# Kernel tuning notes

Hardware: AMD Instinct MI355X
Metric: run time of the kernel (lower is better)

The kernel has to match this reference:

```python
import jax, jax.numpy as jnp
import numpy as np

EPS = 1e-8  # matches PairwiseCosine eps clamp


def setup_inputs() -> dict:
    key = jax.random.key(0)
    k1, k2, k3 = jax.random.split(key, 3)
    B, N, M, D = 8, 2048, 2048, 256
    desc_src = jax.random.normal(k1, (B, N, D), dtype=jnp.float32)
    desc_dst = jax.random.normal(k2, (B, M, D), dtype=jnp.float32)
    points_dst = jax.random.uniform(k3, (B, M, 2), dtype=jnp.float32)
    return {"desc_src": desc_src, "desc_dst": desc_dst, "points_dst": points_dst}


def reference(desc_src, desc_dst, points_dst):
    # Pairwise cosine similarity: [B, N, M]
    xx = jnp.linalg.norm(desc_src, axis=-1, keepdims=True)          # [B, N, 1]
    yy = jnp.linalg.norm(desc_dst, axis=-1, keepdims=True)          # [B, M, 1]
    xy = jnp.einsum('bnd,bmd->bnm', desc_src, desc_dst)             # [B, N, M]
    sim = xy / jnp.maximum(xx * jnp.swapaxes(yy, 1, 2), EPS)
    # Best match per source descriptor
    confidence = jnp.max(sim, axis=2)                               # [B, N]
    idx = jnp.argmax(sim, axis=2)                                   # [B, N]
    # Gather matched destination points: [B, N, 2]
    matched = jnp.take_along_axis(points_dst, idx[:, :, None], axis=1)
    return (matched, confidence)
```

## Files before the change

kernel.cpp:

```cpp
#include <hip/hip_runtime.h>
#include <stdint.h>

constexpr int Bq = 8, Nq = 2048, Mq = 2048, Dq = 256;
constexpr int TILE = 128;
constexpr int KC = 32;
constexpr int NCH = Dq / KC;
constexpr int LDS_S = 40;

typedef float f32x4 __attribute__((ext_vector_type(4)));
typedef _Float16 f16x8 __attribute__((ext_vector_type(8)));
typedef __fp16 fp16x2 __attribute__((ext_vector_type(2)));

__device__ __forceinline__ uint32_t f2sortable(float f) {
  uint32_t u = __float_as_uint(f);
  return (u & 0x80000000u) ? ~u : (u | 0x80000000u);
}
__device__ __forceinline__ float sortable2f(uint32_t s) {
  uint32_t u = (s & 0x80000000u) ? (s ^ 0x80000000u) : ~s;
  return __uint_as_float(u);
}

__device__ __forceinline__ void load16(float* d, const float* __restrict__ p) {
  *(float4*)&d[0]  = *(const float4*)(p + 0);
  *(float4*)&d[4]  = *(const float4*)(p + 4);
  *(float4*)&d[8]  = *(const float4*)(p + 8);
  *(float4*)&d[12] = *(const float4*)(p + 12);
}

__device__ __forceinline__ void split8(const float* x, f16x8* hi, f16x8* lo,
                                       float& sq) {
  union { f16x8 v; fp16x2 p[4]; } H, L;
#pragma unroll
  for (int j = 0; j < 4; ++j) {
    float x0 = x[2 * j], x1 = x[2 * j + 1];
    sq = fmaf(x0, x0, sq);
    sq = fmaf(x1, x1, sq);
    float h0 = __uint_as_float(__float_as_uint(x0) & 0xFFFFE000u);
    float h1 = __uint_as_float(__float_as_uint(x1) & 0xFFFFE000u);
    H.p[j] = __builtin_amdgcn_cvt_pkrtz(h0, h1);
    L.p[j] = __builtin_amdgcn_cvt_pkrtz(x0 - h0, x1 - h1);
  }
  *hi = H.v;
  *lo = L.v;
}

__global__ __launch_bounds__(256, 3)
void simmax_kernel(const float* __restrict__ src, const float* __restrict__ dst,
                   unsigned long long* __restrict__ best) {
  __shared__ _Float16 Ah[TILE][LDS_S], Al[TILE][LDS_S];
  __shared__ _Float16 Bh[TILE][LDS_S], Bl[TILE][LDS_S];
  __shared__ float invnx_s[TILE], invny_s[TILE];

  const int b = blockIdx.z, nt = blockIdx.y, mt = blockIdx.x;
  const int tid = threadIdx.x;
  const int lane = tid & 63;
  const int wave = tid >> 6;
  const int wy = wave >> 1, wx = wave & 1;
  const int ln15 = lane & 15, lq = lane >> 4;

  const int sr = tid >> 1;
  const int sk = (tid & 1) * 16;
  const float* Ag = src + ((size_t)(b * Nq + nt * TILE + sr)) * Dq + sk;
  const float* Bg = dst + ((size_t)(b * Mq + mt * TILE + sr)) * Dq + sk;

  f32x4 acc[4][4];
#pragma unroll
  for (int i = 0; i < 4; ++i)
#pragma unroll
    for (int j = 0; j < 4; ++j) acc[i][j] = (f32x4){0.f, 0.f, 0.f, 0.f};
  float sqa = 0.f, sqb = 0.f;

  float av[16], bv[16];
  load16(av, Ag);
  load16(bv, Bg);

  for (int c = 0; c < NCH; ++c) {
    f16x8 ah2[2], al2[2], bh2[2], bl2[2];
    split8(&av[0], &ah2[0], &al2[0], sqa);
    split8(&av[8], &ah2[1], &al2[1], sqa);
    split8(&bv[0], &bh2[0], &bl2[0], sqb);
    split8(&bv[8], &bh2[1], &bl2[1], sqb);
    __syncthreads();
    *(f16x8*)&Ah[sr][sk]     = ah2[0];
    *(f16x8*)&Ah[sr][sk + 8] = ah2[1];
    *(f16x8*)&Al[sr][sk]     = al2[0];
    *(f16x8*)&Al[sr][sk + 8] = al2[1];
    *(f16x8*)&Bh[sr][sk]     = bh2[0];
    *(f16x8*)&Bh[sr][sk + 8] = bh2[1];
    *(f16x8*)&Bl[sr][sk]     = bl2[0];
    *(f16x8*)&Bl[sr][sk + 8] = bl2[1];
    __syncthreads();

    if (c + 1 < NCH) {
      load16(av, Ag + (c + 1) * KC);
      load16(bv, Bg + (c + 1) * KC);
    }

    f16x8 bhf[4], blf[4];
#pragma unroll
    for (int ct = 0; ct < 4; ++ct) {
      int rowb = wx * 64 + ct * 16 + ln15;
      bhf[ct] = *(const f16x8*)&Bh[rowb][lq * 8];
      blf[ct] = *(const f16x8*)&Bl[rowb][lq * 8];
    }
#pragma unroll
    for (int rt = 0; rt < 4; ++rt) {
      int rowa = wy * 64 + rt * 16 + ln15;
      f16x8 ahf = *(const f16x8*)&Ah[rowa][lq * 8];
      f16x8 alf = *(const f16x8*)&Al[rowa][lq * 8];
#pragma unroll
      for (int ct = 0; ct < 4; ++ct) {
        acc[rt][ct] = __builtin_amdgcn_mfma_f32_16x16x32_f16(ahf, bhf[ct], acc[rt][ct], 0, 0, 0);
        acc[rt][ct] = __builtin_amdgcn_mfma_f32_16x16x32_f16(ahf, blf[ct], acc[rt][ct], 0, 0, 0);
        acc[rt][ct] = __builtin_amdgcn_mfma_f32_16x16x32_f16(alf, bhf[ct], acc[rt][ct], 0, 0, 0);
      }
    }
  }

  sqa += __shfl_xor(sqa, 1);
  sqb += __shfl_xor(sqb, 1);
  if ((tid & 1) == 0) {
    invnx_s[sr] = 1.0f / sqrtf(sqa);
    invny_s[sr] = 1.0f / sqrtf(sqb);
  }
  __syncthreads();

  float invny[4];
#pragma unroll
  for (int ct = 0; ct < 4; ++ct) invny[ct] = invny_s[wx * 64 + ct * 16 + ln15];

#pragma unroll
  for (int rt = 0; rt < 4; ++rt) {
#pragma unroll
    for (int reg = 0; reg < 4; ++reg) {
      float bq = -1e30f;
      int bc = 0x7FFFFFFF;
#pragma unroll
      for (int ct = 0; ct < 4; ++ct) {
        float q = acc[rt][ct][reg] * invny[ct];
        int cg = mt * TILE + wx * 64 + ct * 16 + ln15;
        if (q > bq || (q == bq && cg < bc)) { bq = q; bc = cg; }
      }
#pragma unroll
      for (int m = 1; m <= 8; m <<= 1) {
        float q2 = __shfl_xor(bq, m);
        int c2 = __shfl_xor(bc, m);
        if (q2 > bq || (q2 == bq && c2 < bc)) { bq = q2; bc = c2; }
      }
      if (ln15 == 0) {
        int rloc = wy * 64 + rt * 16 + lq * 4 + reg;
        float conf = bq * invnx_s[rloc];
        unsigned long long p =
            ((unsigned long long)(f2sortable(conf) ^ 0x80000000u) << 32) |
            (uint32_t)(~(uint32_t)bc);
        atomicMax((long long*)&best[(size_t)b * Nq + nt * TILE + rloc],
                  (long long)p);
      }
    }
  }
}

__global__ void finalize_kernel(const unsigned long long* __restrict__ best,
                                const float* __restrict__ pts,
                                float* __restrict__ out) {
  int i = blockIdx.x * blockDim.x + threadIdx.x;
  if (i >= Bq * Nq) return;
  unsigned long long p = best[i];
  uint32_t s = (uint32_t)(p >> 32) ^ 0x80000000u;
  int idx = (int)(~(uint32_t)(p & 0xFFFFFFFFull));
  float conf = sortable2f(s);
  int b = i / Nq;
  const float* q = pts + ((size_t)b * Mq + (size_t)idx) * 2;
  out[(size_t)i * 2 + 0] = q[0];
  out[(size_t)i * 2 + 1] = q[1];
  out[(size_t)(Bq * Nq) * 2 + i] = conf;
}

extern "C" void kernel_launch(void* const* d_in, const int* in_sizes, int n_in,
                              void* d_out, int out_size, void* d_ws, size_t ws_size,
                              hipStream_t stream) {
  const float* src = (const float*)d_in[0];
  const float* dst = (const float*)d_in[1];
  const float* pts = (const float*)d_in[2];
  float* out = (float*)d_out;

  unsigned long long* best = (unsigned long long*)d_ws;

  {
    dim3 grid(Mq / TILE, Nq / TILE, Bq);
    simmax_kernel<<<grid, 256, 0, stream>>>(src, dst, best);
  }
  {
    int blocks = (Bq * Nq + 255) / 256;
    finalize_kernel<<<blocks, 256, 0, stream>>>(best, pts, out);
  }
}
```

Baseline: 150.2 us.

## Precompute fp16 hi/lo splits and norms in separate kernel, load via global_load_lds

```diff
diff --git a/kernel.cpp b/kernel.cpp
--- a/kernel.cpp
+++ b/kernel.cpp
@@ -5,12 +5,20 @@
 constexpr int TILE = 128;
 constexpr int KC = 32;
 constexpr int NCH = Dq / KC;
-constexpr int LDS_S = 40;
+constexpr size_t ROWS = (size_t)Bq * Nq;
+constexpr size_t ARR = ROWS * Dq;
 
 typedef float f32x4 __attribute__((ext_vector_type(4)));
 typedef _Float16 f16x8 __attribute__((ext_vector_type(8)));
 typedef __fp16 fp16x2 __attribute__((ext_vector_type(2)));
 
+typedef const __attribute__((address_space(1))) void* as1_t;
+typedef __attribute__((address_space(3))) void* as3_t;
+
+__device__ __forceinline__ void gl_lds16(const void* g, void* l) {
+  __builtin_amdgcn_global_load_lds((as1_t)g, (as3_t)l, 16, 0, 0);
+}
+
 __device__ __forceinline__ uint32_t f2sortable(float f) {
   uint32_t u = __float_as_uint(f);
   return (u & 0x80000000u) ? ~u : (u | 0x80000000u);
@@ -20,36 +28,48 @@
   return __uint_as_float(u);
 }
 
-__device__ __forceinline__ void load16(float* d, const float* __restrict__ p) {
-  *(float4*)&d[0]  = *(const float4*)(p + 0);
-  *(float4*)&d[4]  = *(const float4*)(p + 4);
-  *(float4*)&d[8]  = *(const float4*)(p + 8);
-  *(float4*)&d[12] = *(const float4*)(p + 12);
-}
-
-__device__ __forceinline__ void split8(const float* x, f16x8* hi, f16x8* lo,
-                                       float& sq) {
-  union { f16x8 v; fp16x2 p[4]; } H, L;
-#pragma unroll
-  for (int j = 0; j < 4; ++j) {
+__global__ __launch_bounds__(256)
+void split_kernel(const float* __restrict__ src, const float* __restrict__ dst,
+                  uint16_t* __restrict__ Ahg, uint16_t* __restrict__ Alg,
+                  uint16_t* __restrict__ Bhg, uint16_t* __restrict__ Blg,
+                  float* __restrict__ inv_ns, float* __restrict__ inv_nd) {
+  int w = blockIdx.x * 4 + (threadIdx.x >> 6);
+  int lane = threadIdx.x & 63;
+  bool isB = w >= (int)ROWS;
+  int row = isB ? (w - (int)ROWS) : w;
+  const float* p = (isB ? dst : src) + (size_t)row * Dq + lane * 4;
+  float4 v = *(const float4*)p;
+  float x[4] = {v.x, v.y, v.z, v.w};
+  float sq = 0.f;
+  union { fp16x2 p2[2]; uint2 u; } H, L;
+#pragma unroll
+  for (int j = 0; j < 2; ++j) {
     float x0 = x[2 * j], x1 = x[2 * j + 1];
     sq = fmaf(x0, x0, sq);
     sq = fmaf(x1, x1, sq);
     float h0 = __uint_as_float(__float_as_uint(x0) & 0xFFFFE000u);
     float h1 = __uint_as_float(__float_as_uint(x1) & 0xFFFFE000u);
-    H.p[j] = __builtin_amdgcn_cvt_pkrtz(h0, h1);
-    L.p[j] = __builtin_amdgcn_cvt_pkrtz(x0 - h0, x1 - h1);
-  }
-  *hi = H.v;
-  *lo = L.v;
-}
-
-__global__ __launch_bounds__(256, 3)
-void simmax_kernel(const float* __restrict__ src, const float* __restrict__ dst,
+    H.p2[j] = __builtin_amdgcn_cvt_pkrtz(h0, h1);
+    L.p2[j] = __builtin_amdgcn_cvt_pkrtz(x0 - h0, x1 - h1);
+  }
+  uint16_t* hp = (isB ? Bhg : Ahg) + (size_t)row * Dq + lane * 4;
+  uint16_t* lp = (isB ? Blg : Alg) + (size_t)row * Dq + lane * 4;
+  *(uint2*)hp = H.u;
+  *(uint2*)lp = L.u;
+#pragma unroll
+  for (int m = 32; m >= 1; m >>= 1) sq += __shfl_xor(sq, m);
+  if (lane == 0) {
+    float inv = 1.0f / sqrtf(sq);
+    (isB ? inv_nd : inv_ns)[row] = inv;
+  }
+}
+
+__global__ __launch_bounds__(256, 4)
+void simmax_kernel(const uint16_t* __restrict__ Ahg, const uint16_t* __restrict__ Alg,
+                   const uint16_t* __restrict__ Bhg, const uint16_t* __restrict__ Blg,
+                   const float* __restrict__ inv_ns, const float* __restrict__ inv_nd,
                    unsigned long long* __restrict__ best) {
-  __shared__ _Float16 Ah[TILE][LDS_S], Al[TILE][LDS_S];
-  __shared__ _Float16 Bh[TILE][LDS_S], Bl[TILE][LDS_S];
-  __shared__ float invnx_s[TILE], invny_s[TILE];
+  __shared__ __align__(16) _Float16 lds[4][TILE][KC];
 
   const int b = blockIdx.z, nt = blockIdx.y, mt = blockIdx.x;
   const int tid = threadIdx.x;
@@ -58,56 +78,39 @@
   const int wy = wave >> 1, wx = wave & 1;
   const int ln15 = lane & 15, lq = lane >> 4;
 
-  const int sr = tid >> 1;
-  const int sk = (tid & 1) * 16;
-  const float* Ag = src + ((size_t)(b * Nq + nt * TILE + sr)) * Dq + sk;
-  const float* Bg = dst + ((size_t)(b * Mq + mt * TILE + sr)) * Dq + sk;
+  const uint16_t* garr = (wave == 0) ? Ahg : (wave == 1) ? Alg
+                        : (wave == 2) ? Bhg : Blg;
+  const int rowg0 = (wave < 2) ? (b * Nq + nt * TILE) : (b * Mq + mt * TILE);
+  const int q = (lane & 3) ^ ((lane >> 3) & 3);
+  const uint16_t* gbase = garr + ((size_t)(rowg0 + (lane >> 2)) * Dq + q * 8);
 
   f32x4 acc[4][4];
 #pragma unroll
   for (int i = 0; i < 4; ++i)
 #pragma unroll
     for (int j = 0; j < 4; ++j) acc[i][j] = (f32x4){0.f, 0.f, 0.f, 0.f};
-  float sqa = 0.f, sqb = 0.f;
-
-  float av[16], bv[16];
-  load16(av, Ag);
-  load16(bv, Bg);
+
+  const int sl = (lq ^ ((ln15 >> 1) & 3)) * 8;
 
   for (int c = 0; c < NCH; ++c) {
-    f16x8 ah2[2], al2[2], bh2[2], bl2[2];
-    split8(&av[0], &ah2[0], &al2[0], sqa);
-    split8(&av[8], &ah2[1], &al2[1], sqa);
-    split8(&bv[0], &bh2[0], &bl2[0], sqb);
-    split8(&bv[8], &bh2[1], &bl2[1], sqb);
     __syncthreads();
-    *(f16x8*)&Ah[sr][sk]     = ah2[0];
-    *(f16x8*)&Ah[sr][sk + 8] = ah2[1];
-    *(f16x8*)&Al[sr][sk]     = al2[0];
-    *(f16x8*)&Al[sr][sk + 8] = al2[1];
-    *(f16x8*)&Bh[sr][sk]     = bh2[0];
-    *(f16x8*)&Bh[sr][sk + 8] = bh2[1];
-    *(f16x8*)&Bl[sr][sk]     = bl2[0];
-    *(f16x8*)&Bl[sr][sk + 8] = bl2[1];
+#pragma unroll
+    for (int t = 0; t < 8; ++t)
+      gl_lds16(gbase + (size_t)(16 * t) * Dq + c * KC, &lds[wave][16 * t][0]);
     __syncthreads();
-
-    if (c + 1 < NCH) {
-      load16(av, Ag + (c + 1) * KC);
-      load16(bv, Bg + (c + 1) * KC);
-    }
 
     f16x8 bhf[4], blf[4];
 #pragma unroll
     for (int ct = 0; ct < 4; ++ct) {
       int rowb = wx * 64 + ct * 16 + ln15;
-      bhf[ct] = *(const f16x8*)&Bh[rowb][lq * 8];
-      blf[ct] = *(const f16x8*)&Bl[rowb][lq * 8];
+      bhf[ct] = *(const f16x8*)&lds[2][rowb][sl];
+      blf[ct] = *(const f16x8*)&lds[3][rowb][sl];
     }
 #pragma unroll
     for (int rt = 0; rt < 4; ++rt) {
       int rowa = wy * 64 + rt * 16 + ln15;
-      f16x8 ahf = *(const f16x8*)&Ah[rowa][lq * 8];
-      f16x8 alf = *(const f16x8*)&Al[rowa][lq * 8];
+      f16x8 ahf = *(const f16x8*)&lds[0][rowa][sl];
+      f16x8 alf = *(const f16x8*)&lds[1][rowa][sl];
 #pragma unroll
       for (int ct = 0; ct < 4; ++ct) {
         acc[rt][ct] = __builtin_amdgcn_mfma_f32_16x16x32_f16(ahf, bhf[ct], acc[rt][ct], 0, 0, 0);
@@ -117,17 +120,10 @@
     }
   }
 
-  sqa += __shfl_xor(sqa, 1);
-  sqb += __shfl_xor(sqb, 1);
-  if ((tid & 1) == 0) {
-    invnx_s[sr] = 1.0f / sqrtf(sqa);
-    invny_s[sr] = 1.0f / sqrtf(sqb);
-  }
-  __syncthreads();
-
   float invny[4];
 #pragma unroll
-  for (int ct = 0; ct < 4; ++ct) invny[ct] = invny_s[wx * 64 + ct * 16 + ln15];
+  for (int ct = 0; ct < 4; ++ct)
+    invny[ct] = inv_nd[b * Mq + mt * TILE + wx * 64 + ct * 16 + ln15];
 
 #pragma unroll
   for (int rt = 0; rt < 4; ++rt) {
@@ -137,9 +133,9 @@
       int bc = 0x7FFFFFFF;
 #pragma unroll
       for (int ct = 0; ct < 4; ++ct) {
-        float q = acc[rt][ct][reg] * invny[ct];
+        float qv = acc[rt][ct][reg] * invny[ct];
         int cg = mt * TILE + wx * 64 + ct * 16 + ln15;
-        if (q > bq || (q == bq && cg < bc)) { bq = q; bc = cg; }
+        if (qv > bq || (qv == bq && cg < bc)) { bq = qv; bc = cg; }
       }
 #pragma unroll
       for (int m = 1; m <= 8; m <<= 1) {
@@ -149,7 +145,7 @@
       }
       if (ln15 == 0) {
         int rloc = wy * 64 + rt * 16 + lq * 4 + reg;
-        float conf = bq * invnx_s[rloc];
+        float conf = bq * inv_ns[b * Nq + nt * TILE + rloc];
         unsigned long long p =
             ((unsigned long long)(f2sortable(conf) ^ 0x80000000u) << 32) |
             (uint32_t)(~(uint32_t)bc);
@@ -164,16 +160,16 @@
                                 const float* __restrict__ pts,
                                 float* __restrict__ out) {
   int i = blockIdx.x * blockDim.x + threadIdx.x;
-  if (i >= Bq * Nq) return;
+  if (i >= (int)ROWS) return;
   unsigned long long p = best[i];
   uint32_t s = (uint32_t)(p >> 32) ^ 0x80000000u;
   int idx = (int)(~(uint32_t)(p & 0xFFFFFFFFull));
   float conf = sortable2f(s);
   int b = i / Nq;
-  const float* q = pts + ((size_t)b * Mq + (size_t)idx) * 2;
-  out[(size_t)i * 2 + 0] = q[0];
-  out[(size_t)i * 2 + 1] = q[1];
-  out[(size_t)(Bq * Nq) * 2 + i] = conf;
+  const float* qp = pts + ((size_t)b * Mq + (size_t)idx) * 2;
+  out[(size_t)i * 2 + 0] = qp[0];
+  out[(size_t)i * 2 + 1] = qp[1];
+  out[ROWS * 2 + i] = conf;
 }
 
 extern "C" void kernel_launch(void* const* d_in, const int* in_sizes, int n_in,
@@ -184,14 +180,27 @@
   const float* pts = (const float*)d_in[2];
   float* out = (float*)d_out;
 
-  unsigned long long* best = (unsigned long long*)d_ws;
-
+  char* w = (char*)d_ws;
+  unsigned long long* best = (unsigned long long*)w;
+  uint16_t* Ahg = (uint16_t*)(w + (128 << 10));
+  uint16_t* Alg = Ahg + ARR;
+  uint16_t* Bhg = Alg + ARR;
+  uint16_t* Blg = Bhg + ARR;
+  float* inv_ns = (float*)(Blg + ARR);
+  float* inv_nd = inv_ns + ROWS;
+
+  {
+    int blocks = (int)(2 * ROWS / 4);
+    split_kernel<<<blocks, 256, 0, stream>>>(src, dst, Ahg, Alg, Bhg, Blg,
+                                             inv_ns, inv_nd);
+  }
   {
     dim3 grid(Mq / TILE, Nq / TILE, Bq);
-    simmax_kernel<<<grid, 256, 0, stream>>>(src, dst, best);
+    simmax_kernel<<<grid, 256, 0, stream>>>(Ahg, Alg, Bhg, Blg, inv_ns, inv_nd,
+                                            best);
   }
   {
-    int blocks = (Bq * Nq + 255) / 256;
+    int blocks = ((int)ROWS + 255) / 256;
     finalize_kernel<<<blocks, 256, 0, stream>>>(best, pts, out);
   }
 }
```

Measured after the change: 164.9 us. 9.8% more time.
